# Performance work log

Measured on AMD Instinct MI355X. Metric: run time of the kernel, lower is better.

Reference implementation:

```python
import jax, jax.numpy as jnp
import numpy as np

N_BOOKS = 8
TAU_Q = 5.0

def setup_inputs() -> dict:
    key = jax.random.key(0)
    k1, k2, k3 = jax.random.split(key, 3)
    N, D_in = 65536, 512
    D = 512          # N_books * L_word
    N_words = 256
    x = jax.random.normal(k1, (N, D_in), dtype=jnp.float32)
    # xavier-uniform-like scale for fc weight [D_out, D_in]
    lim_w = float(np.sqrt(6.0 / (D_in + D)))
    W = jax.random.uniform(k2, (D, D_in), dtype=jnp.float32, minval=-lim_w, maxval=lim_w)
    b = jnp.zeros((D,), dtype=jnp.float32)
    lim_c = float(np.sqrt(6.0 / (N_words + D)))
    C = jax.random.uniform(k3, (N_words, D), dtype=jnp.float32, minval=-lim_c, maxval=lim_c)
    return {"x": x, "W": W, "b": b, "C": C}

def reference(x, W, b, C):
    # fc: X = x @ W^T + b  -> [N, D]
    X = x @ W.T + b
    N, D = X.shape
    M = C.shape[0]
    L = D // N_BOOKS
    Xb = X.reshape(N, N_BOOKS, L)          # [N, B, L]
    Cb = C.reshape(M, N_BOOKS, L)          # [M, B, L]
    x2 = jnp.sum(Xb * Xb, axis=-1)[:, :, None]           # [N, B, 1]
    c2 = jnp.sum(Cb * Cb, axis=-1).T[None, :, :]         # [1, B, M]
    xc = jnp.einsum('nbl,mbl->nbm', Xb, Cb)              # [N, B, M]
    dist = x2 + c2 - 2.0 * xc
    soft = jax.nn.softmax(-TAU_Q * dist, axis=-1)        # softmax over codewords
    # weighted codebook sum per book, then concat books -> [N, D]
    Z = jnp.einsum('nbm,mbl->nbl', soft, Cb).reshape(N, D)
    return X, Z
```

## Files before the change

### kernel.cpp

```cpp
#include <hip/hip_runtime.h>
#include <cstdint>
#include <cstddef>

#define N_ROWS   65536
#define D_IN     512
#define D_OUT    512
#define N_WORDS  256
#define N_BOOKS  8
#define TAU      5.0f
#define LOG2E    1.44269504088896340736f

typedef __attribute__((ext_vector_type(8))) short short8;
typedef __attribute__((ext_vector_type(4))) float f32x4;

__device__ __forceinline__ unsigned short f2bf(float f) {
    __bf16 h = (__bf16)f;
    return __builtin_bit_cast(unsigned short, h);
}
__device__ __forceinline__ float bf2f(unsigned short h) {
    unsigned u = ((unsigned)h) << 16;
    return __builtin_bit_cast(float, u);
}

__global__ __launch_bounds__(256) void prep_codebook(
        const float* __restrict__ C, const float* __restrict__ W,
        unsigned short* __restrict__ packA, unsigned short* __restrict__ packB,
        unsigned short* __restrict__ packW, float* __restrict__ nc2) {
    const int gid = blockIdx.x * 256 + threadIdx.x;
    if (gid < 131072) {
        const int i  = gid & 7;
        const int l  = (gid >> 3) & 63;
        const int mf = (gid >> 9) & 15;
        const int ks = (gid >> 13) & 1;
        const int b  = gid >> 14;
        const int row = (l & 15) + 16 * mf;
        const int col = b * 64 + (l >> 4) * 8 + i + 32 * ks;
        packA[gid] = f2bf(C[(size_t)row * D_IN + col]);
    } else if (gid < 262144) {
        const int g   = gid - 131072;
        const int i   = g & 7;
        const int l   = (g >> 3) & 63;
        const int n2  = (g >> 9) & 3;
        const int ks2 = (g >> 11) & 7;
        const int b   = g >> 14;
        const int m   = 32 * ks2 + 16 * (i >> 2) + 4 * (l >> 4) + (i & 3);
        const int col = b * 64 + n2 * 16 + (l & 15);
        packB[g] = f2bf(C[(size_t)m * D_IN + col]);
    } else if (gid < 524288) {
        const int h  = gid - 262144;
        const int i  = h & 7;
        const int l  = (h >> 3) & 63;
        const int cf = (h >> 9) & 7;
        const int kk = (h >> 12) & 15;
        const int bn = h >> 16;
        packW[h] = f2bf(W[(size_t)(bn * 128 + cf * 16 + (l & 15)) * D_IN
                          + kk * 32 + (l >> 4) * 8 + i]);
    } else if (gid < 526336) {
        const int t = gid - 524288;
        const int b = t >> 8, m = t & 255;
        const float* cp = C + (size_t)m * D_IN + b * 64;
        float s = 0.f;
        for (int l = 0; l < 64; ++l) {
            const float v = bf2f(f2bf(cp[l]));
            s = fmaf(v, v, s);
        }
        nc2[t] = -TAU * LOG2E * s;
    }
}

#define ASTR 40

__global__ __launch_bounds__(256) void gemm_fc(
        const float* __restrict__ x, const unsigned short* __restrict__ packW,
        const float* __restrict__ bias, float* __restrict__ X) {
    __shared__ unsigned short Asm[128 * ASTR];

    const int tid = threadIdx.x;
    const int bid = blockIdx.x;
    const int swz = (bid & 7) * 256 + (bid >> 3);
    const int bm = swz >> 2, bn = swz & 3;
    const int n0 = bm * 128, c0 = bn * 128;
    const int lane = tid & 63, w = tid >> 6;
    const int wr = w >> 1, wc = w & 1;
    const int lo = lane & 15, hi = lane >> 4;

    const int sr = tid >> 1;
    const int sf = (tid & 1) << 4;

    f32x4 acc[4][4];
    #pragma unroll
    for (int i = 0; i < 4; ++i)
        #pragma unroll
        for (int j = 0; j < 4; ++j) acc[i][j] = (f32x4){0.f, 0.f, 0.f, 0.f};

    float4 ra[4];
    {
        const float* xa = &x[(size_t)(n0 + sr) * D_IN + sf];
        #pragma unroll
        for (int q = 0; q < 4; ++q)
            ra[q] = *reinterpret_cast<const float4*>(xa + q * 4);
    }

    for (int kk = 0; kk < 16; ++kk) {
        #pragma unroll
        for (int q = 0; q < 4; ++q) {
            ushort4 pa;
            pa.x = f2bf(ra[q].x); pa.y = f2bf(ra[q].y);
            pa.z = f2bf(ra[q].z); pa.w = f2bf(ra[q].w);
            *reinterpret_cast<ushort4*>(&Asm[sr * ASTR + sf + q * 4]) = pa;
        }
        if (kk < 15) {
            const float* xa = &x[(size_t)(n0 + sr) * D_IN + (kk + 1) * 32 + sf];
            #pragma unroll
            for (int q = 0; q < 4; ++q)
                ra[q] = *reinterpret_cast<const float4*>(xa + q * 4);
        }
        short8 bb[4];
        {
            const unsigned short* wp = packW
                + ((size_t)((bn * 16 + kk) * 8 + wc * 4) * 64) * 8;
            #pragma unroll
            for (int fn = 0; fn < 4; ++fn)
                bb[fn] = *reinterpret_cast<const short8*>(wp + ((size_t)fn * 64 + lane) * 8);
        }
        __syncthreads();
        short8 a[4];
        #pragma unroll
        for (int fm = 0; fm < 4; ++fm)
            a[fm] = *reinterpret_cast<const short8*>(&Asm[(wr * 64 + fm * 16 + lo) * ASTR + hi * 8]);
        #pragma unroll
        for (int fm = 0; fm < 4; ++fm)
            #pragma unroll
            for (int fn = 0; fn < 4; ++fn)
                acc[fm][fn] = __builtin_amdgcn_mfma_f32_16x16x32_bf16(
                    a[fm], bb[fn], acc[fm][fn], 0, 0, 0);
        __syncthreads();
    }

    #pragma unroll
    for (int fn = 0; fn < 4; ++fn) {
        const float bv = bias[c0 + wc * 64 + fn * 16 + lo];
        #pragma unroll
        for (int fm = 0; fm < 4; ++fm)
            #pragma unroll
            for (int j = 0; j < 4; ++j)
                X[(size_t)(n0 + wr * 64 + fm * 16 + hi * 4 + j) * D_OUT
                  + c0 + wc * 64 + fn * 16 + lo] = acc[fm][fn][j] + bv;
    }
}

__global__ __launch_bounds__(512, 4) void quant_head(
        const float* __restrict__ X, const unsigned short* __restrict__ packA,
        const unsigned short* __restrict__ packB, const float* __restrict__ nc2g,
        float* __restrict__ Z) {
    __shared__ __attribute__((aligned(16))) unsigned short cbA[16384];
    __shared__ __attribute__((aligned(16))) unsigned short cbB[16384];
    __shared__ float nc2s[256];

    const int tid  = threadIdx.x;
    const int b    = blockIdx.x & 7;
    const int n0   = (blockIdx.x >> 3) * 128;
    const int lane = tid & 63;
    const int w    = tid >> 6;
    const int lo = lane & 15, hi = lane >> 4;
    const int row = n0 + w * 16 + lo;

    const float* xp = X + (size_t)row * D_OUT + b * 64 + hi * 8;
    const float4 rx0 = *reinterpret_cast<const float4*>(xp);
    const float4 rx1 = *reinterpret_cast<const float4*>(xp + 4);
    const float4 rx2 = *reinterpret_cast<const float4*>(xp + 32);
    const float4 rx3 = *reinterpret_cast<const float4*>(xp + 36);

    {
        const float4* gA = reinterpret_cast<const float4*>(packA + (size_t)b * 16384);
        const float4* gB = reinterpret_cast<const float4*>(packB + (size_t)b * 16384);
        float4* sA = reinterpret_cast<float4*>(cbA);
        float4* sB = reinterpret_cast<float4*>(cbB);
        #pragma unroll
        for (int it = 0; it < 4; ++it) {
            sA[it * 512 + tid] = gA[it * 512 + tid];
            sB[it * 512 + tid] = gB[it * 512 + tid];
        }
        if (tid < 256) nc2s[tid] = nc2g[b * 256 + tid];
    }

    short8 xf[2];
    {
        short8 t;
        t[0] = (short)f2bf(rx0.x); t[1] = (short)f2bf(rx0.y);
        t[2] = (short)f2bf(rx0.z); t[3] = (short)f2bf(rx0.w);
        t[4] = (short)f2bf(rx1.x); t[5] = (short)f2bf(rx1.y);
        t[6] = (short)f2bf(rx1.z); t[7] = (short)f2bf(rx1.w);
        xf[0] = t;
        t[0] = (short)f2bf(rx2.x); t[1] = (short)f2bf(rx2.y);
        t[2] = (short)f2bf(rx2.z); t[3] = (short)f2bf(rx2.w);
        t[4] = (short)f2bf(rx3.x); t[5] = (short)f2bf(rx3.y);
        t[6] = (short)f2bf(rx3.z); t[7] = (short)f2bf(rx3.w);
        xf[1] = t;
    }

    __syncthreads();

    f32x4 acc[16];
    #pragma unroll
    for (int mf = 0; mf < 16; ++mf) acc[mf] = (f32x4){0.f, 0.f, 0.f, 0.f};
    #pragma unroll
    for (int ks = 0; ks < 2; ++ks)
        #pragma unroll
        for (int mf = 0; mf < 16; ++mf) {
            const short8 cfr = *reinterpret_cast<const short8*>(
                &cbA[((ks * 16 + mf) * 64 + lane) * 8]);
            acc[mf] = __builtin_amdgcn_mfma_f32_16x16x32_bf16(cfr, xf[ks], acc[mf], 0, 0, 0);
        }

    const float S2 = 2.0f * TAU * LOG2E;
    float s = 0.f;
    #pragma unroll
    for (int mf = 0; mf < 16; ++mf) {
        const f32x4 nv = *reinterpret_cast<const f32x4*>(&nc2s[mf * 16 + hi * 4]);
        const float p0 = exp2f(fmaf(acc[mf][0], S2, nv[0]));
        const float p1 = exp2f(fmaf(acc[mf][1], S2, nv[1]));
        const float p2 = exp2f(fmaf(acc[mf][2], S2, nv[2]));
        const float p3 = exp2f(fmaf(acc[mf][3], S2, nv[3]));
        acc[mf][0] = p0; acc[mf][1] = p1; acc[mf][2] = p2; acc[mf][3] = p3;
        s += (p0 + p1) + (p2 + p3);
    }
    s += __shfl_xor(s, 16, 64);
    s += __shfl_xor(s, 32, 64);
    const float inv = 1.0f / s;

    f32x4 acc2[4];
    #pragma unroll
    for (int n2 = 0; n2 < 4; ++n2) acc2[n2] = (f32x4){0.f, 0.f, 0.f, 0.f};
    #pragma unroll
    for (int ks2 = 0; ks2 < 8; ++ks2) {
        short8 pa;
        pa[0] = (short)f2bf(acc[2 * ks2][0]);     pa[1] = (short)f2bf(acc[2 * ks2][1]);
        pa[2] = (short)f2bf(acc[2 * ks2][2]);     pa[3] = (short)f2bf(acc[2 * ks2][3]);
        pa[4] = (short)f2bf(acc[2 * ks2 + 1][0]); pa[5] = (short)f2bf(acc[2 * ks2 + 1][1]);
        pa[6] = (short)f2bf(acc[2 * ks2 + 1][2]); pa[7] = (short)f2bf(acc[2 * ks2 + 1][3]);
        #pragma unroll
        for (int n2 = 0; n2 < 4; ++n2) {
            const short8 bv = *reinterpret_cast<const short8*>(
                &cbB[((ks2 * 4 + n2) * 64 + lane) * 8]);
            acc2[n2] = __builtin_amdgcn_mfma_f32_16x16x32_bf16(pa, bv, acc2[n2], 0, 0, 0);
        }
    }

    float invr[4];
    #pragma unroll
    for (int j = 0; j < 4; ++j) invr[j] = __shfl(inv, hi * 4 + j, 64);
    #pragma unroll
    for (int n2 = 0; n2 < 4; ++n2)
        #pragma unroll
        for (int j = 0; j < 4; ++j)
            Z[(size_t)(n0 + w * 16 + hi * 4 + j) * D_OUT + b * 64 + n2 * 16 + lo]
                = acc2[n2][j] * invr[j];
}

extern "C" void kernel_launch(void* const* d_in, const int* in_sizes, int n_in,
                              void* d_out, int out_size, void* d_ws, size_t ws_size,
                              hipStream_t stream) {
    const float* x = (const float*)d_in[0];
    const float* W = (const float*)d_in[1];
    const float* b = (const float*)d_in[2];
    const float* C = (const float*)d_in[3];

    float* X = (float*)d_out;
    float* Z = X + (size_t)N_ROWS * D_OUT;

    unsigned short* packA = (unsigned short*)d_ws;
    unsigned short* packB = packA + 131072;
    unsigned short* packW = packB + 131072;
    float*          nc2g  = (float*)(packW + 262144);

    prep_codebook<<<dim3(2056), dim3(256), 0, stream>>>(C, W, packA, packB, packW, nc2g);
    gemm_fc<<<dim3(2048), dim3(256), 0, stream>>>(x, packW, b, X);
    quant_head<<<dim3(N_BOOKS * (N_ROWS / 128)), dim3(512), 0, stream>>>(
        X, packA, packB, nc2g, Z);
}
```

Before: 182.6 us.

## Fuse fc GEMM with per-book soft quantization in one kernel

Merges the fc GEMM and the quant head into a single kernel. Each block computes one 64-column book slice of X for 256 rows, writes it to global memory, and keeps a bf16 copy in shared memory that feeds the codeword-distance and softmax stages directly. This avoids reading X back from global memory and removes one kernel launch. In exchange, every book block re-reads the same x rows, so x traffic grows eightfold. LDS per block also rises, which limits occupancy.

```diff
diff --git a/kernel.cpp b/kernel.cpp
--- a/kernel.cpp
+++ b/kernel.cpp
@@ -50,10 +50,10 @@
         const int h  = gid - 262144;
         const int i  = h & 7;
         const int l  = (h >> 3) & 63;
-        const int cf = (h >> 9) & 7;
-        const int kk = (h >> 12) & 15;
-        const int bn = h >> 16;
-        packW[h] = f2bf(W[(size_t)(bn * 128 + cf * 16 + (l & 15)) * D_IN
+        const int cf = (h >> 9) & 3;
+        const int kk = (h >> 11) & 15;
+        const int b  = h >> 15;
+        packW[h] = f2bf(W[(size_t)(b * 64 + cf * 16 + (l & 15)) * D_IN
                           + kk * 32 + (l >> 4) * 8 + i]);
     } else if (gid < 526336) {
         const int t = gid - 524288;
@@ -68,108 +68,29 @@
     }
 }
 
-#define ASTR 40
-
-__global__ __launch_bounds__(256) void gemm_fc(
+#define XSTR 72
+
+__global__ __launch_bounds__(512, 2) void fused_fc_quant(
         const float* __restrict__ x, const unsigned short* __restrict__ packW,
-        const float* __restrict__ bias, float* __restrict__ X) {
-    __shared__ unsigned short Asm[128 * ASTR];
-
-    const int tid = threadIdx.x;
-    const int bid = blockIdx.x;
-    const int swz = (bid & 7) * 256 + (bid >> 3);
-    const int bm = swz >> 2, bn = swz & 3;
-    const int n0 = bm * 128, c0 = bn * 128;
-    const int lane = tid & 63, w = tid >> 6;
-    const int wr = w >> 1, wc = w & 1;
-    const int lo = lane & 15, hi = lane >> 4;
-
-    const int sr = tid >> 1;
-    const int sf = (tid & 1) << 4;
-
-    f32x4 acc[4][4];
-    #pragma unroll
-    for (int i = 0; i < 4; ++i)
-        #pragma unroll
-        for (int j = 0; j < 4; ++j) acc[i][j] = (f32x4){0.f, 0.f, 0.f, 0.f};
-
-    float4 ra[4];
-    {
-        const float* xa = &x[(size_t)(n0 + sr) * D_IN + sf];
-        #pragma unroll
-        for (int q = 0; q < 4; ++q)
-            ra[q] = *reinterpret_cast<const float4*>(xa + q * 4);
-    }
-
-    for (int kk = 0; kk < 16; ++kk) {
-        #pragma unroll
-        for (int q = 0; q < 4; ++q) {
-            ushort4 pa;
-            pa.x = f2bf(ra[q].x); pa.y = f2bf(ra[q].y);
-            pa.z = f2bf(ra[q].z); pa.w = f2bf(ra[q].w);
-            *reinterpret_cast<ushort4*>(&Asm[sr * ASTR + sf + q * 4]) = pa;
-        }
-        if (kk < 15) {
-            const float* xa = &x[(size_t)(n0 + sr) * D_IN + (kk + 1) * 32 + sf];
-            #pragma unroll
-            for (int q = 0; q < 4; ++q)
-                ra[q] = *reinterpret_cast<const float4*>(xa + q * 4);
-        }
-        short8 bb[4];
-        {
-            const unsigned short* wp = packW
-                + ((size_t)((bn * 16 + kk) * 8 + wc * 4) * 64) * 8;
-            #pragma unroll
-            for (int fn = 0; fn < 4; ++fn)
-                bb[fn] = *reinterpret_cast<const short8*>(wp + ((size_t)fn * 64 + lane) * 8);
-        }
-        __syncthreads();
-        short8 a[4];
-        #pragma unroll
-        for (int fm = 0; fm < 4; ++fm)
-            a[fm] = *reinterpret_cast<const short8*>(&Asm[(wr * 64 + fm * 16 + lo) * ASTR + hi * 8]);
-        #pragma unroll
-        for (int fm = 0; fm < 4; ++fm)
-            #pragma unroll
-            for (int fn = 0; fn < 4; ++fn)
-                acc[fm][fn] = __builtin_amdgcn_mfma_f32_16x16x32_bf16(
-                    a[fm], bb[fn], acc[fm][fn], 0, 0, 0);
-        __syncthreads();
-    }
-
-    #pragma unroll
-    for (int fn = 0; fn < 4; ++fn) {
-        const float bv = bias[c0 + wc * 64 + fn * 16 + lo];
-        #pragma unroll
-        for (int fm = 0; fm < 4; ++fm)
-            #pragma unroll
-            for (int j = 0; j < 4; ++j)
-                X[(size_t)(n0 + wr * 64 + fm * 16 + hi * 4 + j) * D_OUT
-                  + c0 + wc * 64 + fn * 16 + lo] = acc[fm][fn][j] + bv;
-    }
-}
-
-__global__ __launch_bounds__(512, 4) void quant_head(
-        const float* __restrict__ X, const unsigned short* __restrict__ packA,
-        const unsigned short* __restrict__ packB, const float* __restrict__ nc2g,
-        float* __restrict__ Z) {
+        const float* __restrict__ bias,
+        const unsigned short* __restrict__ packA,
+        const unsigned short* __restrict__ packB,
+        const float* __restrict__ nc2g,
+        float* __restrict__ X, float* __restrict__ Z) {
     __shared__ __attribute__((aligned(16))) unsigned short cbA[16384];
     __shared__ __attribute__((aligned(16))) unsigned short cbB[16384];
+    __shared__ __attribute__((aligned(16))) unsigned short XtAsm[256 * XSTR];
     __shared__ float nc2s[256];
 
     const int tid  = threadIdx.x;
     const int b    = blockIdx.x & 7;
-    const int n0   = (blockIdx.x >> 3) * 128;
+    const int n0   = (blockIdx.x >> 3) * 256;
     const int lane = tid & 63;
     const int w    = tid >> 6;
     const int lo = lane & 15, hi = lane >> 4;
-    const int row = n0 + w * 16 + lo;
-
-    const float* xp = X + (size_t)row * D_OUT + b * 64 + hi * 8;
-    const float4 rx0 = *reinterpret_cast<const float4*>(xp);
-    const float4 rx1 = *reinterpret_cast<const float4*>(xp + 4);
-    const float4 rx2 = *reinterpret_cast<const float4*>(xp + 32);
-    const float4 rx3 = *reinterpret_cast<const float4*>(xp + 36);
+
+    const int sr = tid >> 1;
+    const int sf = (tid & 1) << 5;
 
     {
         const float4* gA = reinterpret_cast<const float4*>(packA + (size_t)b * 16384);
@@ -184,78 +105,141 @@
         if (tid < 256) nc2s[tid] = nc2g[b * 256 + tid];
     }
 
-    short8 xf[2];
+    f32x4 acc[2][4];
+    #pragma unroll
+    for (int fm = 0; fm < 2; ++fm)
+        #pragma unroll
+        for (int fn = 0; fn < 4; ++fn) acc[fm][fn] = (f32x4){0.f, 0.f, 0.f, 0.f};
+
+    float4 ra[8];
     {
-        short8 t;
-        t[0] = (short)f2bf(rx0.x); t[1] = (short)f2bf(rx0.y);
-        t[2] = (short)f2bf(rx0.z); t[3] = (short)f2bf(rx0.w);
-        t[4] = (short)f2bf(rx1.x); t[5] = (short)f2bf(rx1.y);
-        t[6] = (short)f2bf(rx1.z); t[7] = (short)f2bf(rx1.w);
-        xf[0] = t;
-        t[0] = (short)f2bf(rx2.x); t[1] = (short)f2bf(rx2.y);
-        t[2] = (short)f2bf(rx2.z); t[3] = (short)f2bf(rx2.w);
-        t[4] = (short)f2bf(rx3.x); t[5] = (short)f2bf(rx3.y);
-        t[6] = (short)f2bf(rx3.z); t[7] = (short)f2bf(rx3.w);
-        xf[1] = t;
-    }
-
-    __syncthreads();
-
-    f32x4 acc[16];
+        const float* xa = &x[(size_t)(n0 + sr) * D_IN + sf];
+        #pragma unroll
+        for (int q = 0; q < 8; ++q)
+            ra[q] = *reinterpret_cast<const float4*>(xa + q * 4);
+    }
+
+    for (int t = 0; t < 8; ++t) {
+        #pragma unroll
+        for (int q = 0; q < 8; ++q) {
+            ushort4 pa;
+            pa.x = f2bf(ra[q].x); pa.y = f2bf(ra[q].y);
+            pa.z = f2bf(ra[q].z); pa.w = f2bf(ra[q].w);
+            *reinterpret_cast<ushort4*>(&XtAsm[sr * XSTR + sf + q * 4]) = pa;
+        }
+        if (t < 7) {
+            const float* xa = &x[(size_t)(n0 + sr) * D_IN + (t + 1) * 64 + sf];
+            #pragma unroll
+            for (int q = 0; q < 8; ++q)
+                ra[q] = *reinterpret_cast<const float4*>(xa + q * 4);
+        }
+        short8 bb[2][4];
+        #pragma unroll
+        for (int ks = 0; ks < 2; ++ks)
+            #pragma unroll
+            for (int cf = 0; cf < 4; ++cf)
+                bb[ks][cf] = *reinterpret_cast<const short8*>(
+                    packW + ((size_t)(((b * 16 + 2 * t + ks) * 4) + cf) * 64 + lane) * 8);
+        __syncthreads();
+        short8 a[2][2];
+        #pragma unroll
+        for (int fm = 0; fm < 2; ++fm)
+            #pragma unroll
+            for (int ks = 0; ks < 2; ++ks)
+                a[fm][ks] = *reinterpret_cast<const short8*>(
+                    &XtAsm[(w * 32 + fm * 16 + lo) * XSTR + ks * 32 + hi * 8]);
+        #pragma unroll
+        for (int ks = 0; ks < 2; ++ks)
+            #pragma unroll
+            for (int fm = 0; fm < 2; ++fm)
+                #pragma unroll
+                for (int cf = 0; cf < 4; ++cf)
+                    acc[fm][cf] = __builtin_amdgcn_mfma_f32_16x16x32_bf16(
+                        a[fm][ks], bb[ks][cf], acc[fm][cf], 0, 0, 0);
+        __syncthreads();
+    }
+
     #pragma unroll
-    for (int mf = 0; mf < 16; ++mf) acc[mf] = (f32x4){0.f, 0.f, 0.f, 0.f};
-    #pragma unroll
-    for (int ks = 0; ks < 2; ++ks)
+    for (int fn = 0; fn < 4; ++fn) {
+        const float bv = bias[b * 64 + fn * 16 + lo];
+        #pragma unroll
+        for (int fm = 0; fm < 2; ++fm)
+            #pragma unroll
+            for (int j = 0; j < 4; ++j) {
+                const float v = acc[fm][fn][j] + bv;
+                const int r = w * 32 + fm * 16 + hi * 4 + j;
+                X[(size_t)(n0 + r) * D_OUT + b * 64 + fn * 16 + lo] = v;
+                XtAsm[r * XSTR + fn * 16 + lo] = f2bf(v);
+            }
+    }
+
+    const float S2 = 2.0f * TAU * LOG2E;
+    for (int h = 0; h < 2; ++h) {
+        const int rb = w * 32 + h * 16;
+        const short8 xf0 = *reinterpret_cast<const short8*>(
+            &XtAsm[(rb + lo) * XSTR + hi * 8]);
+        const short8 xf1 = *reinterpret_cast<const short8*>(
+            &XtAsm[(rb + lo) * XSTR + 32 + hi * 8]);
+
+        f32x4 qa[16];
+        #pragma unroll
+        for (int mf = 0; mf < 16; ++mf) qa[mf] = (f32x4){0.f, 0.f, 0.f, 0.f};
         #pragma unroll
         for (int mf = 0; mf < 16; ++mf) {
             const short8 cfr = *reinterpret_cast<const short8*>(
-                &cbA[((ks * 16 + mf) * 64 + lane) * 8]);
-            acc[mf] = __builtin_amdgcn_mfma_f32_16x16x32_bf16(cfr, xf[ks], acc[mf], 0, 0, 0);
-        }
-
-    const float S2 = 2.0f * TAU * LOG2E;
-    float s = 0.f;
-    #pragma unroll
-    for (int mf = 0; mf < 16; ++mf) {
-        const f32x4 nv = *reinterpret_cast<const f32x4*>(&nc2s[mf * 16 + hi * 4]);
-        const float p0 = exp2f(fmaf(acc[mf][0], S2, nv[0]));
-        const float p1 = exp2f(fmaf(acc[mf][1], S2, nv[1]));
-        const float p2 = exp2f(fmaf(acc[mf][2], S2, nv[2]));
-        const float p3 = exp2f(fmaf(acc[mf][3], S2, nv[3]));
-        acc[mf][0] = p0; acc[mf][1] = p1; acc[mf][2] = p2; acc[mf][3] = p3;
-        s += (p0 + p1) + (p2 + p3);
-    }
-    s += __shfl_xor(s, 16, 64);
-    s += __shfl_xor(s, 32, 64);
-    const float inv = 1.0f / s;
-
-    f32x4 acc2[4];
-    #pragma unroll
-    for (int n2 = 0; n2 < 4; ++n2) acc2[n2] = (f32x4){0.f, 0.f, 0.f, 0.f};
-    #pragma unroll
-    for (int ks2 = 0; ks2 < 8; ++ks2) {
-        short8 pa;
-        pa[0] = (short)f2bf(acc[2 * ks2][0]);     pa[1] = (short)f2bf(acc[2 * ks2][1]);
-        pa[2] = (short)f2bf(acc[2 * ks2][2]);     pa[3] = (short)f2bf(acc[2 * ks2][3]);
-        pa[4] = (short)f2bf(acc[2 * ks2 + 1][0]); pa[5] = (short)f2bf(acc[2 * ks2 + 1][1]);
-        pa[6] = (short)f2bf(acc[2 * ks2 + 1][2]); pa[7] = (short)f2bf(acc[2 * ks2 + 1][3]);
-        #pragma unroll
-        for (int n2 = 0; n2 < 4; ++n2) {
-            const short8 bv = *reinterpret_cast<const short8*>(
-                &cbB[((ks2 * 4 + n2) * 64 + lane) * 8]);
-            acc2[n2] = __builtin_amdgcn_mfma_f32_16x16x32_bf16(pa, bv, acc2[n2], 0, 0, 0);
-        }
-    }
-
-    float invr[4];
-    #pragma unroll
-    for (int j = 0; j < 4; ++j) invr[j] = __shfl(inv, hi * 4 + j, 64);
-    #pragma unroll
-    for (int n2 = 0; n2 < 4; ++n2)
-        #pragma unroll
-        for (int j = 0; j < 4; ++j)
-            Z[(size_t)(n0 + w * 16 + hi * 4 + j) * D_OUT + b * 64 + n2 * 16 + lo]
-                = acc2[n2][j] * invr[j];
+                &cbA[(mf * 64 + lane) * 8]);
+            qa[mf] = __builtin_amdgcn_mfma_f32_16x16x32_bf16(cfr, xf0, qa[mf], 0, 0, 0);
+        }
+        #pragma unroll
+        for (int mf = 0; mf < 16; ++mf) {
+            const short8 cfr = *reinterpret_cast<const short8*>(
+                &cbA[((16 + mf) * 64 + lane) * 8]);
+            qa[mf] = __builtin_amdgcn_mfma_f32_16x16x32_bf16(cfr, xf1, qa[mf], 0, 0, 0);
+        }
+
+        float s = 0.f;
+        #pragma unroll
+        for (int mf = 0; mf < 16; ++mf) {
+            const f32x4 nv = *reinterpret_cast<const f32x4*>(&nc2s[mf * 16 + hi * 4]);
+            const float p0 = exp2f(fmaf(qa[mf][0], S2, nv[0]));
+            const float p1 = exp2f(fmaf(qa[mf][1], S2, nv[1]));
+            const float p2 = exp2f(fmaf(qa[mf][2], S2, nv[2]));
+            const float p3 = exp2f(fmaf(qa[mf][3], S2, nv[3]));
+            qa[mf][0] = p0; qa[mf][1] = p1; qa[mf][2] = p2; qa[mf][3] = p3;
+            s += (p0 + p1) + (p2 + p3);
+        }
+        s += __shfl_xor(s, 16, 64);
+        s += __shfl_xor(s, 32, 64);
+        const float inv = 1.0f / s;
+
+        f32x4 acc2[4];
+        #pragma unroll
+        for (int n2 = 0; n2 < 4; ++n2) acc2[n2] = (f32x4){0.f, 0.f, 0.f, 0.f};
+        #pragma unroll
+        for (int ks2 = 0; ks2 < 8; ++ks2) {
+            short8 pa;
+            pa[0] = (short)f2bf(qa[2 * ks2][0]);     pa[1] = (short)f2bf(qa[2 * ks2][1]);
+            pa[2] = (short)f2bf(qa[2 * ks2][2]);     pa[3] = (short)f2bf(qa[2 * ks2][3]);
+            pa[4] = (short)f2bf(qa[2 * ks2 + 1][0]); pa[5] = (short)f2bf(qa[2 * ks2 + 1][1]);
+            pa[6] = (short)f2bf(qa[2 * ks2 + 1][2]); pa[7] = (short)f2bf(qa[2 * ks2 + 1][3]);
+            #pragma unroll
+            for (int n2 = 0; n2 < 4; ++n2) {
+                const short8 bv = *reinterpret_cast<const short8*>(
+                    &cbB[((ks2 * 4 + n2) * 64 + lane) * 8]);
+                acc2[n2] = __builtin_amdgcn_mfma_f32_16x16x32_bf16(pa, bv, acc2[n2], 0, 0, 0);
+            }
+        }
+
+        float invr[4];
+        #pragma unroll
+        for (int j = 0; j < 4; ++j) invr[j] = __shfl(inv, hi * 4 + j, 64);
+        #pragma unroll
+        for (int n2 = 0; n2 < 4; ++n2)
+            #pragma unroll
+            for (int j = 0; j < 4; ++j)
+                Z[(size_t)(n0 + rb + hi * 4 + j) * D_OUT + b * 64 + n2 * 16 + lo]
+                    = acc2[n2][j] * invr[j];
+    }
 }
 
 extern "C" void kernel_launch(void* const* d_in, const int* in_sizes, int n_in,
@@ -275,7 +259,6 @@
     float*          nc2g  = (float*)(packW + 262144);
 
     prep_codebook<<<dim3(2056), dim3(256), 0, stream>>>(C, W, packA, packB, packW, nc2g);
-    gemm_fc<<<dim3(2048), dim3(256), 0, stream>>>(x, packW, b, X);
-    quant_head<<<dim3(N_BOOKS * (N_ROWS / 128)), dim3(512), 0, stream>>>(
-        X, packA, packB, nc2g, Z);
-}
+    fused_fc_quant<<<dim3(N_BOOKS * (N_ROWS / 256)), dim3(512), 0, stream>>>(
+        x, packW, b, packA, packB, nc2g, X, Z);
+}
```

Result: slower. 278.5 us (+52.5%).

## Enlarge GEMM and quant tiles to 256 rows, stage W in LDS, XCD-aware mapping

Applied to the files above, without the earlier changes.

gemm_fc now uses 512-thread blocks covering 256 rows, staging the packed W slice in shared memory once per k-step so eight waves share it instead of each reading it from global memory. quant_head processes 256 rows per block, two 16-row halves per wave, so the codebook LDS fill is amortised over twice the rows. Both kernels remap block ids so consecutive row tiles land on the same XCD, which should improve L2 locality. The cost is larger blocks with more LDS and registers, which may lower occupancy, plus an extra barrier-protected shared-memory store of W each iteration.

```diff
diff --git a/kernel.cpp b/kernel.cpp
--- a/kernel.cpp
+++ b/kernel.cpp
@@ -70,16 +70,19 @@
 
 #define ASTR 40
 
-__global__ __launch_bounds__(256) void gemm_fc(
+__global__ __launch_bounds__(512, 4) void gemm_fc(
         const float* __restrict__ x, const unsigned short* __restrict__ packW,
         const float* __restrict__ bias, float* __restrict__ X) {
-    __shared__ unsigned short Asm[128 * ASTR];
+    __shared__ unsigned short Asm[256 * ASTR];
+    __shared__ __attribute__((aligned(16))) unsigned short Wsm[4096];
 
     const int tid = threadIdx.x;
     const int bid = blockIdx.x;
-    const int swz = (bid & 7) * 256 + (bid >> 3);
-    const int bm = swz >> 2, bn = swz & 3;
-    const int n0 = bm * 128, c0 = bn * 128;
+    const int xcd = bid & 7;
+    const int idx = bid >> 3;
+    const int bm  = xcd * 32 + (idx >> 2);
+    const int bn  = idx & 3;
+    const int n0 = bm * 256, c0 = bn * 128;
     const int lane = tid & 63, w = tid >> 6;
     const int wr = w >> 1, wc = w & 1;
     const int lo = lane & 15, hi = lane >> 4;
@@ -101,7 +104,11 @@
             ra[q] = *reinterpret_cast<const float4*>(xa + q * 4);
     }
 
+    const float4* gW = reinterpret_cast<const float4*>(packW);
+    float4* sW = reinterpret_cast<float4*>(Wsm);
+
     for (int kk = 0; kk < 16; ++kk) {
+        sW[tid] = gW[(size_t)(bn * 16 + kk) * 512 + tid];
         #pragma unroll
         for (int q = 0; q < 4; ++q) {
             ushort4 pa;
@@ -115,37 +122,34 @@
             for (int q = 0; q < 4; ++q)
                 ra[q] = *reinterpret_cast<const float4*>(xa + q * 4);
         }
-        short8 bb[4];
-        {
-            const unsigned short* wp = packW
-                + ((size_t)((bn * 16 + kk) * 8 + wc * 4) * 64) * 8;
-            #pragma unroll
-            for (int fn = 0; fn < 4; ++fn)
-                bb[fn] = *reinterpret_cast<const short8*>(wp + ((size_t)fn * 64 + lane) * 8);
-        }
         __syncthreads();
-        short8 a[4];
+        short8 a[4], bb[4];
         #pragma unroll
         for (int fm = 0; fm < 4; ++fm)
-            a[fm] = *reinterpret_cast<const short8*>(&Asm[(wr * 64 + fm * 16 + lo) * ASTR + hi * 8]);
+            a[fm] = *reinterpret_cast<const short8*>(
+                &Asm[(wr * 64 + fm * 16 + lo) * ASTR + hi * 8]);
+        #pragma unroll
+        for (int cf = 0; cf < 4; ++cf)
+            bb[cf] = *reinterpret_cast<const short8*>(
+                &Wsm[((wc * 4 + cf) * 64 + lane) * 8]);
         #pragma unroll
         for (int fm = 0; fm < 4; ++fm)
             #pragma unroll
-            for (int fn = 0; fn < 4; ++fn)
-                acc[fm][fn] = __builtin_amdgcn_mfma_f32_16x16x32_bf16(
-                    a[fm], bb[fn], acc[fm][fn], 0, 0, 0);
+            for (int cf = 0; cf < 4; ++cf)
+                acc[fm][cf] = __builtin_amdgcn_mfma_f32_16x16x32_bf16(
+                    a[fm], bb[cf], acc[fm][cf], 0, 0, 0);
         __syncthreads();
     }
 
     #pragma unroll
-    for (int fn = 0; fn < 4; ++fn) {
-        const float bv = bias[c0 + wc * 64 + fn * 16 + lo];
+    for (int cf = 0; cf < 4; ++cf) {
+        const float bv = bias[c0 + wc * 64 + cf * 16 + lo];
         #pragma unroll
         for (int fm = 0; fm < 4; ++fm)
             #pragma unroll
             for (int j = 0; j < 4; ++j)
                 X[(size_t)(n0 + wr * 64 + fm * 16 + hi * 4 + j) * D_OUT
-                  + c0 + wc * 64 + fn * 16 + lo] = acc[fm][fn][j] + bv;
+                  + c0 + wc * 64 + cf * 16 + lo] = acc[fm][cf][j] + bv;
     }
 }
 
@@ -158,18 +162,24 @@
     __shared__ float nc2s[256];
 
     const int tid  = threadIdx.x;
-    const int b    = blockIdx.x & 7;
-    const int n0   = (blockIdx.x >> 3) * 128;
+    const int bid  = blockIdx.x;
+    const int xcd = bid & 7;
+    const int idx = bid >> 3;
+    const int b   = idx & 7;
+    const int n0  = (xcd * 32 + (idx >> 3)) * 256;
     const int lane = tid & 63;
     const int w    = tid >> 6;
     const int lo = lane & 15, hi = lane >> 4;
-    const int row = n0 + w * 16 + lo;
-
-    const float* xp = X + (size_t)row * D_OUT + b * 64 + hi * 8;
-    const float4 rx0 = *reinterpret_cast<const float4*>(xp);
-    const float4 rx1 = *reinterpret_cast<const float4*>(xp + 4);
-    const float4 rx2 = *reinterpret_cast<const float4*>(xp + 32);
-    const float4 rx3 = *reinterpret_cast<const float4*>(xp + 36);
+
+    float4 rx[2][4];
+    #pragma unroll
+    for (int h = 0; h < 2; ++h) {
+        const float* xp = X + (size_t)(n0 + w * 32 + h * 16 + lo) * D_OUT + b * 64 + hi * 8;
+        rx[h][0] = *reinterpret_cast<const float4*>(xp);
+        rx[h][1] = *reinterpret_cast<const float4*>(xp + 4);
+        rx[h][2] = *reinterpret_cast<const float4*>(xp + 32);
+        rx[h][3] = *reinterpret_cast<const float4*>(xp + 36);
+    }
 
     {
         const float4* gA = reinterpret_cast<const float4*>(packA + (size_t)b * 16384);
@@ -184,78 +194,81 @@
         if (tid < 256) nc2s[tid] = nc2g[b * 256 + tid];
     }
 
-    short8 xf[2];
-    {
-        short8 t;
-        t[0] = (short)f2bf(rx0.x); t[1] = (short)f2bf(rx0.y);
-        t[2] = (short)f2bf(rx0.z); t[3] = (short)f2bf(rx0.w);
-        t[4] = (short)f2bf(rx1.x); t[5] = (short)f2bf(rx1.y);
-        t[6] = (short)f2bf(rx1.z); t[7] = (short)f2bf(rx1.w);
-        xf[0] = t;
-        t[0] = (short)f2bf(rx2.x); t[1] = (short)f2bf(rx2.y);
-        t[2] = (short)f2bf(rx2.z); t[3] = (short)f2bf(rx2.w);
-        t[4] = (short)f2bf(rx3.x); t[5] = (short)f2bf(rx3.y);
-        t[6] = (short)f2bf(rx3.z); t[7] = (short)f2bf(rx3.w);
-        xf[1] = t;
-    }
+    short8 xf[2][2];
+    #pragma unroll
+    for (int h = 0; h < 2; ++h)
+        #pragma unroll
+        for (int ks = 0; ks < 2; ++ks) {
+            const float4 v0 = rx[h][ks * 2];
+            const float4 v1 = rx[h][ks * 2 + 1];
+            short8 t;
+            t[0] = (short)f2bf(v0.x); t[1] = (short)f2bf(v0.y);
+            t[2] = (short)f2bf(v0.z); t[3] = (short)f2bf(v0.w);
+            t[4] = (short)f2bf(v1.x); t[5] = (short)f2bf(v1.y);
+            t[6] = (short)f2bf(v1.z); t[7] = (short)f2bf(v1.w);
+            xf[h][ks] = t;
+        }
 
     __syncthreads();
 
-    f32x4 acc[16];
-    #pragma unroll
-    for (int mf = 0; mf < 16; ++mf) acc[mf] = (f32x4){0.f, 0.f, 0.f, 0.f};
-    #pragma unroll
-    for (int ks = 0; ks < 2; ++ks)
+    const float S2 = 2.0f * TAU * LOG2E;
+    for (int h = 0; h < 2; ++h) {
+        f32x4 qa[16];
+        #pragma unroll
+        for (int mf = 0; mf < 16; ++mf) qa[mf] = (f32x4){0.f, 0.f, 0.f, 0.f};
+        #pragma unroll
+        for (int ks = 0; ks < 2; ++ks)
+            #pragma unroll
+            for (int mf = 0; mf < 16; ++mf) {
+                const short8 cfr = *reinterpret_cast<const short8*>(
+                    &cbA[((ks * 16 + mf) * 64 + lane) * 8]);
+                qa[mf] = __builtin_amdgcn_mfma_f32_16x16x32_bf16(
+                    cfr, xf[h][ks], qa[mf], 0, 0, 0);
+            }
+
+        float s = 0.f;
         #pragma unroll
         for (int mf = 0; mf < 16; ++mf) {
-            const short8 cfr = *reinterpret_cast<const short8*>(
-                &cbA[((ks * 16 + mf) * 64 + lane) * 8]);
-            acc[mf] = __builtin_amdgcn_mfma_f32_16x16x32_bf16(cfr, xf[ks], acc[mf], 0, 0, 0);
-        }
-
-    const float S2 = 2.0f * TAU * LOG2E;
-    float s = 0.f;
-    #pragma unroll
-    for (int mf = 0; mf < 16; ++mf) {
-        const f32x4 nv = *reinterpret_cast<const f32x4*>(&nc2s[mf * 16 + hi * 4]);
-        const float p0 = exp2f(fmaf(acc[mf][0], S2, nv[0]));
-        const float p1 = exp2f(fmaf(acc[mf][1], S2, nv[1]));
-        const float p2 = exp2f(fmaf(acc[mf][2], S2, nv[2]));
-        const float p3 = exp2f(fmaf(acc[mf][3], S2, nv[3]));
-        acc[mf][0] = p0; acc[mf][1] = p1; acc[mf][2] = p2; acc[mf][3] = p3;
-        s += (p0 + p1) + (p2 + p3);
-    }
-    s += __shfl_xor(s, 16, 64);
-    s += __shfl_xor(s, 32, 64);
-    const float inv = 1.0f / s;
-
-    f32x4 acc2[4];
-    #pragma unroll
-    for (int n2 = 0; n2 < 4; ++n2) acc2[n2] = (f32x4){0.f, 0.f, 0.f, 0.f};
-    #pragma unroll
-    for (int ks2 = 0; ks2 < 8; ++ks2) {
-        short8 pa;
-        pa[0] = (short)f2bf(acc[2 * ks2][0]);     pa[1] = (short)f2bf(acc[2 * ks2][1]);
-        pa[2] = (short)f2bf(acc[2 * ks2][2]);     pa[3] = (short)f2bf(acc[2 * ks2][3]);
-        pa[4] = (short)f2bf(acc[2 * ks2 + 1][0]); pa[5] = (short)f2bf(acc[2 * ks2 + 1][1]);
-        pa[6] = (short)f2bf(acc[2 * ks2 + 1][2]); pa[7] = (short)f2bf(acc[2 * ks2 + 1][3]);
-        #pragma unroll
-        for (int n2 = 0; n2 < 4; ++n2) {
-            const short8 bv = *reinterpret_cast<const short8*>(
-                &cbB[((ks2 * 4 + n2) * 64 + lane) * 8]);
-            acc2[n2] = __builtin_amdgcn_mfma_f32_16x16x32_bf16(pa, bv, acc2[n2], 0, 0, 0);
-        }
-    }
-
-    float invr[4];
-    #pragma unroll
-    for (int j = 0; j < 4; ++j) invr[j] = __shfl(inv, hi * 4 + j, 64);
-    #pragma unroll
-    for (int n2 = 0; n2 < 4; ++n2)
-        #pragma unroll
-        for (int j = 0; j < 4; ++j)
-            Z[(size_t)(n0 + w * 16 + hi * 4 + j) * D_OUT + b * 64 + n2 * 16 + lo]
-                = acc2[n2][j] * invr[j];
+            const f32x4 nv = *reinterpret_cast<const f32x4*>(&nc2s[mf * 16 + hi * 4]);
+            const float p0 = exp2f(fmaf(qa[mf][0], S2, nv[0]));
+            const float p1 = exp2f(fmaf(qa[mf][1], S2, nv[1]));
+            const float p2 = exp2f(fmaf(qa[mf][2], S2, nv[2]));
+            const float p3 = exp2f(fmaf(qa[mf][3], S2, nv[3]));
+            qa[mf][0] = p0; qa[mf][1] = p1; qa[mf][2] = p2; qa[mf][3] = p3;
+            s += (p0 + p1) + (p2 + p3);
+        }
+        s += __shfl_xor(s, 16, 64);
+        s += __shfl_xor(s, 32, 64);
+        const float inv = 1.0f / s;
+
+        f32x4 acc2[4];
+        #pragma unroll
+        for (int n2 = 0; n2 < 4; ++n2) acc2[n2] = (f32x4){0.f, 0.f, 0.f, 0.f};
+        #pragma unroll
+        for (int ks2 = 0; ks2 < 8; ++ks2) {
+            short8 pa;
+            pa[0] = (short)f2bf(qa[2 * ks2][0]);     pa[1] = (short)f2bf(qa[2 * ks2][1]);
+            pa[2] = (short)f2bf(qa[2 * ks2][2]);     pa[3] = (short)f2bf(qa[2 * ks2][3]);
+            pa[4] = (short)f2bf(qa[2 * ks2 + 1][0]); pa[5] = (short)f2bf(qa[2 * ks2 + 1][1]);
+            pa[6] = (short)f2bf(qa[2 * ks2 + 1][2]); pa[7] = (short)f2bf(qa[2 * ks2 + 1][3]);
+            #pragma unroll
+            for (int n2 = 0; n2 < 4; ++n2) {
+                const short8 bv = *reinterpret_cast<const short8*>(
+                    &cbB[((ks2 * 4 + n2) * 64 + lane) * 8]);
+                acc2[n2] = __builtin_amdgcn_mfma_f32_16x16x32_bf16(pa, bv, acc2[n2], 0, 0, 0);
+            }
+        }
+
+        float invr[4];
+        #pragma unroll
+        for (int j = 0; j < 4; ++j) invr[j] = __shfl(inv, hi * 4 + j, 64);
+        #pragma unroll
+        for (int n2 = 0; n2 < 4; ++n2)
+            #pragma unroll
+            for (int j = 0; j < 4; ++j)
+                Z[(size_t)(n0 + w * 32 + h * 16 + hi * 4 + j) * D_OUT + b * 64 + n2 * 16 + lo]
+                    = acc2[n2][j] * invr[j];
+    }
 }
 
 extern "C" void kernel_launch(void* const* d_in, const int* in_sizes, int n_in,
@@ -275,7 +288,7 @@
     float*          nc2g  = (float*)(packW + 262144);
 
     prep_codebook<<<dim3(2056), dim3(256), 0, stream>>>(C, W, packA, packB, packW, nc2g);
-    gemm_fc<<<dim3(2048), dim3(256), 0, stream>>>(x, packW, b, X);
-    quant_head<<<dim3(N_BOOKS * (N_ROWS / 128)), dim3(512), 0, stream>>>(
+    gemm_fc<<<dim3(1024), dim3(512), 0, stream>>>(x, packW, b, X);
+    quant_head<<<dim3(N_BOOKS * (N_ROWS / 256)), dim3(512), 0, stream>>>(
         X, packA, packB, nc2g, Z);
 }
```

Result: faster. 172.0 us (-5.8%).
